# Kernel tuning notes

Measured on AMD Instinct MI355X. Metric: run time of the kernel, lower is better.

## Reference

```python
import jax, jax.numpy as jnp
import numpy as np

N_NODES = 100000
N_EDGES = 3200000


def setup_inputs() -> dict:
    key = jax.random.key(0)
    k1, k2, k3, k4 = jax.random.split(key, 4)
    x = jax.random.normal(k1, (N_NODES, 128), dtype=jnp.float32)
    edge_index = jax.random.randint(k2, (2, N_EDGES), 0, N_NODES, dtype=jnp.int64)
    W1 = jax.random.normal(k3, (128, 16), dtype=jnp.float32) * 0.1
    b1 = jnp.zeros((16,), dtype=jnp.float32)
    W2 = jax.random.normal(k4, (16, 1), dtype=jnp.float32) * 0.1
    b2 = jnp.zeros((1,), dtype=jnp.float32)
    return {"x": x, "edge_index": edge_index, "W1": W1, "b1": b1, "W2": W2, "b2": b2}


def _gcn_conv(h, row, col, norm, b, n):
    # message = h[src] * norm, scatter-add into dst (PyG source_to_target flow)
    msg = h[row] * norm[:, None]
    out = jax.ops.segment_sum(msg, col, num_segments=n)
    return out + b


def reference(x, edge_index, W1, b1, W2, b2):
    n = x.shape[0]
    loops = jnp.arange(n, dtype=edge_index.dtype)
    # GCN adds self-loops with weight 1
    row = jnp.concatenate([edge_index[0], loops])
    col = jnp.concatenate([edge_index[1], loops])
    ew = jnp.ones(row.shape[0], dtype=x.dtype)
    deg = jax.ops.segment_sum(ew, col, num_segments=n)
    dinv = jnp.where(deg > 0, deg ** -0.5, 0.0).astype(x.dtype)
    norm = dinv[row] * dinv[col]

    h = _gcn_conv(x @ W1, row, col, norm, b1, n)  # [N,16]
    h = jax.nn.relu(h)
    # dropout p=0.2 is identity in eval mode
    h = _gcn_conv(h @ W2, row, col, norm, b2, n)  # [N,1]
    return jax.nn.sigmoid(h).squeeze(-1)  # [N]
```

## Files before the change

### kernel.cpp

```cpp
#include <hip/hip_runtime.h>
#include <hip/hip_fp16.h>
#include <cstdint>


#define F_IN 128
#define F_HID 16
#define PB 1024
#define PT 8192
#define NBMAX 512
#define CAPMAX 15104

__global__ __launch_bounds__(PB) void partition_kernel(
    const int* __restrict__ row, const int* __restrict__ col,
    int* __restrict__ cursor,
    int* __restrict__ ping,
    int capB, int NB, int n_edges) {
    __shared__ int sh_hist[NBMAX];
    __shared__ int sh_scan[NBMAX];
    __shared__ int sh_cur[NBMAX];
    __shared__ int sh_base[NBMAX];
    __shared__ int sh_wsum[16];
    __shared__ int sh_packed[PT];
    __shared__ unsigned short sh_bkt[PT];

    int t = threadIdx.x;
    int lane = t & 63;
    int wv = t >> 6;
    int ntiles = (n_edges + PT - 1) / PT;
    bool vec_ok = ((n_edges & 3) == 0);

    for (int tile = blockIdx.x; tile < ntiles; tile += gridDim.x) {
        int tbase = tile * PT;
        int tcnt = min(PT, n_edges - tbase);

        if (t < NBMAX) sh_hist[t] = 0;
        __syncthreads();

        int e0 = tbase + t * 8;
        int pk[8], bb[8];
        if (vec_ok && e0 + 8 <= n_edges) {
            int4 a0 = *(const int4*)(row + e0);
            int4 a1 = *(const int4*)(row + e0 + 4);
            int4 c0 = *(const int4*)(col + e0);
            int4 c1 = *(const int4*)(col + e0 + 4);
            int rr[8] = {a0.x, a0.y, a0.z, a0.w, a1.x, a1.y, a1.z, a1.w};
            int cc[8] = {c0.x, c0.y, c0.z, c0.w, c1.x, c1.y, c1.z, c1.w};
#pragma unroll
            for (int k = 0; k < 8; k++) {
                bb[k] = cc[k] >> 8;
                pk[k] = rr[k] | ((cc[k] & 255) << 17);
                atomicAdd(&sh_hist[bb[k]], 1);
            }
        } else {
#pragma unroll
            for (int k = 0; k < 8; k++) {
                int e = e0 + k;
                bb[k] = -1;
                if (e < n_edges) {
                    int r = row[e];
                    int c = col[e];
                    bb[k] = c >> 8;
                    pk[k] = r | ((c & 255) << 17);
                    atomicAdd(&sh_hist[bb[k]], 1);
                }
            }
        }
        __syncthreads();

        {
            int v = (t < NBMAX) ? sh_hist[t] : 0;
            int incl = v;
#pragma unroll
            for (int off = 1; off < 64; off <<= 1) {
                int u = __shfl_up(incl, off, 64);
                if (lane >= off) incl += u;
            }
            if (lane == 63) sh_wsum[wv] = incl;
            __syncthreads();
            if (t < 16) {
                int s = sh_wsum[t];
#pragma unroll
                for (int off = 1; off < 16; off <<= 1) {
                    int u = __shfl_up(s, off, 16);
                    if (t >= off) s += u;
                }
                sh_wsum[t] = s;
            }
            __syncthreads();
            int wexcl = (wv > 0) ? sh_wsum[wv - 1] : 0;
            if (t < NBMAX) sh_scan[t] = incl + wexcl;
        }
        __syncthreads();

        if (t < NBMAX) {
            int h = sh_hist[t];
            sh_cur[t] = sh_scan[t] - h;
            sh_base[t] = (h > 0 && t < NB) ? atomicAdd(&cursor[t], h) : 0;
        }
        __syncthreads();

#pragma unroll
        for (int k = 0; k < 8; k++) {
            if (bb[k] >= 0) {
                int p = atomicAdd(&sh_cur[bb[k]], 1);
                sh_packed[p] = pk[k];
                sh_bkt[p] = (unsigned short)bb[k];
            }
        }
        __syncthreads();

#pragma unroll
        for (int k = 0; k < 8; k++) {
            int p = t + k * PB;
            if (p < tcnt) {
                int b = sh_bkt[p];
                int off = p - (sh_scan[b] - sh_hist[b]);
                int gp = sh_base[b] + off;
                if (gp < capB) ping[(size_t)b * capB + gp] = sh_packed[p];
            }
        }
        __syncthreads();
    }
}

__global__ __launch_bounds__(PB) void deg_gemm1_kernel(
    const int* __restrict__ cursor, const int* __restrict__ ping,
    const float* __restrict__ x, const float* __restrict__ W1,
    int* __restrict__ cnt, int* __restrict__ rowptr,
    __half* __restrict__ h1p, int capB, int n) {
    __shared__ float sW[F_IN * F_HID];
    __shared__ int hist[256];
    __shared__ int wsum[4];

    int b = blockIdx.x, t = threadIdx.x;
    int lane = t & 63;
    int wv = t >> 6;

    for (int i = t; i < F_IN * F_HID; i += PB) sW[i] = W1[i];
    if (t < 256) hist[t] = 0;
    __syncthreads();

    int cb = min(cursor[b], capB);
    const int* src = ping + (size_t)b * capB;
    for (int i = t; i < cb; i += PB) {
        atomicAdd(&hist[(src[i] >> 17) & 255], 1);
    }
    __syncthreads();

    {
        int h = (t < 256) ? hist[t] : 0;
        int incl = h;
#pragma unroll
        for (int off = 1; off < 64; off <<= 1) {
            int u = __shfl_up(incl, off, 64);
            if (lane >= off) incl += u;
        }
        if (t < 256 && lane == 63) wsum[wv] = incl;
        __syncthreads();
        if (t < 4) {
            int s = wsum[t];
#pragma unroll
            for (int off = 1; off < 4; off <<= 1) {
                int u = __shfl_up(s, off, 4);
                if (t >= off) s += u;
            }
            wsum[t] = s;
        }
        __syncthreads();
        if (t < 256) {
            int g = b * 256 + t;
            if (g < n) {
                int wexcl = (wv > 0) ? wsum[wv - 1] : 0;
                cnt[g] = h;
                rowptr[g] = b * capB + (incl + wexcl - h);
            }
        }
    }

    int sub = t >> 2;
    int node = b * 256 + sub;
    if (node >= n) return;
    int jq = (t & 3) * 4;

    const float4* xr = (const float4*)(x + (size_t)node * F_IN);
    float a0 = 0.0f, a1 = 0.0f, a2 = 0.0f, a3 = 0.0f;

#pragma unroll 4
    for (int k4 = 0; k4 < F_IN / 4; k4++) {
        float4 xv = xr[k4];
        const float* w0 = &sW[(k4 * 4 + 0) * F_HID + jq];
        const float* w1 = &sW[(k4 * 4 + 1) * F_HID + jq];
        const float* w2 = &sW[(k4 * 4 + 2) * F_HID + jq];
        const float* w3 = &sW[(k4 * 4 + 3) * F_HID + jq];
        a0 += xv.x * w0[0] + xv.y * w1[0] + xv.z * w2[0] + xv.w * w3[0];
        a1 += xv.x * w0[1] + xv.y * w1[1] + xv.z * w2[1] + xv.w * w3[1];
        a2 += xv.x * w0[2] + xv.y * w1[2] + xv.z * w2[2] + xv.w * w3[2];
        a3 += xv.x * w0[3] + xv.y * w1[3] + xv.z * w2[3] + xv.w * w3[3];
    }

    float d = rsqrtf((float)hist[sub] + 1.0f);
    __half2 hv[2];
    hv[0] = __floats2half2_rn(a0 * d, a1 * d);
    hv[1] = __floats2half2_rn(a2 * d, a3 * d);
    *(float2*)(h1p + (size_t)node * F_HID + jq) = *(float2*)&hv[0];
}

__global__ __launch_bounds__(PB) void sort_gather1(
    const int* __restrict__ cursor, const int* __restrict__ ping,
    const int* __restrict__ cnt, const int* __restrict__ rowptr,
    const __half* __restrict__ h1p, const float* __restrict__ b1,
    const float* __restrict__ W2, float* __restrict__ sp,
    int* __restrict__ pong, int capB, int n) {
    extern __shared__ int B[];
    __shared__ int s_excl[256];
    __shared__ int s_h[256];
    __shared__ int cur[256];

    int b = blockIdx.x, t = threadIdx.x;

    if (t < 256) {
        int g = b * 256 + t;
        int h = (g < n) ? cnt[g] : 0;
        int excl = (g < n) ? (rowptr[g] - b * capB) : 0;
        s_h[t] = h;
        s_excl[t] = excl;
        cur[t] = excl;
    }
    __syncthreads();

    int cb = min(cursor[b], capB);
    const int* src = ping + (size_t)b * capB;

    for (int i = t; i < cb; i += PB) {
        int v = src[i];
        int p = atomicAdd(&cur[(v >> 17) & 255], 1);
        B[p] = v & 131071;
    }
    __syncthreads();

    for (int i = t; i < cb; i += PB) {
        pong[(size_t)b * capB + i] = B[i];
    }

    int l = t & 7;
    for (int j = t >> 3; j < 256; j += (PB >> 3)) {
        int g = b * 256 + j;
        if (g >= n) continue;
        int h = s_h[j];
        int base = s_excl[j];
        int end = base + h;

        float ax = 0.0f, ay = 0.0f;
        for (; base + 8 <= end; base += 8) {
#pragma unroll
            for (int m = 0; m < 8; m++) {
                int rm = B[base + m];
                float2 f = __half22float2(*(const __half2*)(h1p + (size_t)rm * F_HID + 2 * l));
                ax += f.x; ay += f.y;
            }
        }
        for (int m = 0; m < end - base; m++) {
            int rm = B[base + m];
            float2 f = __half22float2(*(const __half2*)(h1p + (size_t)rm * F_HID + 2 * l));
            ax += f.x; ay += f.y;
        }

        float dc = rsqrtf((float)h + 1.0f);
        float2 fs = __half22float2(*(const __half2*)(h1p + (size_t)g * F_HID + 2 * l));
        float v0 = (ax + fs.x) * dc + b1[2 * l];
        float v1 = (ay + fs.y) * dc + b1[2 * l + 1];
        v0 = fmaxf(v0, 0.0f);
        v1 = fmaxf(v1, 0.0f);
        float tt = v0 * W2[2 * l] + v1 * W2[2 * l + 1];
        tt += __shfl_xor(tt, 1, 8);
        tt += __shfl_xor(tt, 2, 8);
        tt += __shfl_xor(tt, 4, 8);
        if (l == 0) sp[g] = tt * dc;
    }
}

__global__ __launch_bounds__(256) void gather2_kernel(const int* __restrict__ rowptr,
                                                      const int* __restrict__ cnt,
                                                      const int* __restrict__ eidx,
                                                      const float* __restrict__ sp,
                                                      const float* __restrict__ b2,
                                                      float* __restrict__ out, int n) {
    int g = (blockIdx.x * 256 + threadIdx.x) >> 4;
    int lane = threadIdx.x & 15;
    if (g >= n) return;
    int start = rowptr[g];
    int end = start + cnt[g];

    float acc = 0.0f;
    for (int e = start + lane; e < end; e += 16) {
        acc += sp[eidx[e]];
    }
    acc += __shfl_xor(acc, 1, 16);
    acc += __shfl_xor(acc, 2, 16);
    acc += __shfl_xor(acc, 4, 16);
    acc += __shfl_xor(acc, 8, 16);
    if (lane == 0) {
        float v = (acc + sp[g]) * rsqrtf((float)cnt[g] + 1.0f) + b2[0];
        out[g] = 1.0f / (1.0f + __expf(-v));
    }
}

__global__ void bucket_scatter_kernel(const int* __restrict__ row,
                                      const int* __restrict__ col,
                                      int* __restrict__ cnt,
                                      int* __restrict__ eidx,
                                      int cap, int n_edges) {
    int e = blockIdx.x * blockDim.x + threadIdx.x;
    if (e < n_edges) {
        int c = col[e];
        int p = atomicAdd(&cnt[c], 1);
        if (p < cap) eidx[(size_t)c * cap + p] = row[e];
    }
}

__global__ __launch_bounds__(256) void gemm1f_kernel(const float* __restrict__ x,
                                                     const float* __restrict__ W1,
                                                     const int* __restrict__ cnt,
                                                     float* __restrict__ h1p, int n) {
    __shared__ float sW[F_IN * F_HID];
    int tid = threadIdx.x;
    for (int i = tid; i < F_IN * F_HID; i += 256) sW[i] = W1[i];
    __syncthreads();
    int node = blockIdx.x * 256 + tid;
    if (node >= n) return;
    const float4* xr = (const float4*)(x + (size_t)node * F_IN);
    float acc[F_HID];
#pragma unroll
    for (int j = 0; j < F_HID; j++) acc[j] = 0.0f;
#pragma unroll 4
    for (int k4 = 0; k4 < F_IN / 4; k4++) {
        float4 xv = xr[k4];
        const float* w0 = &sW[(k4 * 4 + 0) * F_HID];
        const float* w1 = &sW[(k4 * 4 + 1) * F_HID];
        const float* w2 = &sW[(k4 * 4 + 2) * F_HID];
        const float* w3 = &sW[(k4 * 4 + 3) * F_HID];
#pragma unroll
        for (int j = 0; j < F_HID; j++) {
            acc[j] += xv.x * w0[j] + xv.y * w1[j] + xv.z * w2[j] + xv.w * w3[j];
        }
    }
    float d = rsqrtf((float)cnt[node] + 1.0f);
    float4* outp = (float4*)(h1p + (size_t)node * F_HID);
    outp[0] = make_float4(acc[0] * d, acc[1] * d, acc[2] * d, acc[3] * d);
    outp[1] = make_float4(acc[4] * d, acc[5] * d, acc[6] * d, acc[7] * d);
    outp[2] = make_float4(acc[8] * d, acc[9] * d, acc[10] * d, acc[11] * d);
    outp[3] = make_float4(acc[12] * d, acc[13] * d, acc[14] * d, acc[15] * d);
}

__global__ __launch_bounds__(256) void fb_gather1_kernel(const int* __restrict__ cnt,
                                                         const int* __restrict__ eidx,
                                                         const float* __restrict__ h1p,
                                                         const float* __restrict__ b1,
                                                         const float* __restrict__ W2,
                                                         float* __restrict__ sp,
                                                         int cap, int n) {
    int g = (blockIdx.x * 256 + threadIdx.x) >> 4;
    int lane = threadIdx.x & 15;
    if (g >= n) return;
    int start = g * cap;
    int end = start + min(cnt[g], cap);
    float acc = 0.0f;
    for (int base = start; base < end; base += 16) {
        int e = base + lane;
        int r = (e < end) ? eidx[e] : 0;
        int m_cnt = min(16, end - base);
        for (int m = 0; m < m_cnt; m++) {
            int rm = __shfl(r, m, 16);
            acc += h1p[(size_t)rm * F_HID + lane];
        }
    }
    float dc = rsqrtf((float)cnt[g] + 1.0f);
    float v = (acc + h1p[(size_t)g * F_HID + lane]) * dc + b1[lane];
    v = fmaxf(v, 0.0f);
    float t = v * W2[lane];
    t += __shfl_xor(t, 1, 16);
    t += __shfl_xor(t, 2, 16);
    t += __shfl_xor(t, 4, 16);
    t += __shfl_xor(t, 8, 16);
    if (lane == 0) sp[g] = t * dc;
}

__global__ __launch_bounds__(256) void fb_gather2_kernel(const int* __restrict__ cnt,
                                                         const int* __restrict__ eidx,
                                                         const float* __restrict__ sp,
                                                         const float* __restrict__ b2,
                                                         float* __restrict__ out,
                                                         int cap, int n) {
    int g = (blockIdx.x * 256 + threadIdx.x) >> 4;
    int lane = threadIdx.x & 15;
    if (g >= n) return;
    int start = g * cap;
    int end = start + min(cnt[g], cap);
    float acc = 0.0f;
    for (int e = start + lane; e < end; e += 16) {
        acc += sp[eidx[e]];
    }
    acc += __shfl_xor(acc, 1, 16);
    acc += __shfl_xor(acc, 2, 16);
    acc += __shfl_xor(acc, 4, 16);
    acc += __shfl_xor(acc, 8, 16);
    if (lane == 0) {
        float v = (acc + sp[g]) * rsqrtf((float)cnt[g] + 1.0f) + b2[0];
        out[g] = 1.0f / (1.0f + __expf(-v));
    }
}

extern "C" void kernel_launch(void* const* d_in, const int* in_sizes, int n_in,
                              void* d_out, int out_size, void* d_ws, size_t ws_size,
                              hipStream_t stream) {
    const float* x  = (const float*)d_in[0];
    const int*   ei = (const int*)d_in[1];
    const float* W1 = (const float*)d_in[2];
    const float* b1 = (const float*)d_in[3];
    const float* W2 = (const float*)d_in[4];
    const float* b2 = (const float*)d_in[5];
    float* out = (float*)d_out;

    const int n = in_sizes[0] / F_IN;
    const int n_edges = in_sizes[1] / 2;
    const int* row = ei;
    const int* col = ei + n_edges;

    const size_t S = ((size_t)n + 511) & ~(size_t)511;
    const size_t words = ws_size / 4;

    const int B = 256;
    const int gridE = (n_edges + B - 1) / B;
    const int gridN = (n + B - 1) / B;

    const int NB = (n + 255) >> 8;
    int meanB = (NB > 0) ? (n_edges / NB) : 0;
    int capB = ((meanB + meanB / 8 + 1024) + 15) & ~15;
    size_t need_new = 11 * S + (size_t)NBMAX + 2 * (size_t)NB * (size_t)capB;

    if (n <= 131072 && NB <= NBMAX && capB <= CAPMAX && words >= need_new) {
        int*    cnt    = (int*)d_ws;
        int*    cursor = cnt + S;
        int*    rowptr = cursor + NBMAX;
        float*  sp     = (float*)(rowptr + S);
        __half* h1p    = (__half*)(sp + S);
        int*    ping   = (int*)(sp + S) + 8 * S;
        int*    pong   = ping + (size_t)NB * capB;

        hipMemsetAsync(cursor, 0, NBMAX * sizeof(int), stream);
        int ntiles = (n_edges + PT - 1) / PT;
        int pgrid = min(2048, ntiles);
        partition_kernel<<<pgrid, PB, 0, stream>>>(row, col, cursor, ping,
                                                   capB, NB, n_edges);
        deg_gemm1_kernel<<<NB, PB, 0, stream>>>(cursor, ping, x, W1, cnt,
                                                rowptr, h1p, capB, n);
        sort_gather1<<<NB, PB, (size_t)capB * sizeof(int), stream>>>(
            cursor, ping, cnt, rowptr, h1p, b1, W2, sp, pong, capB, n);
        int gridG2 = (n * 16 + B - 1) / B;
        gather2_kernel<<<gridG2, B, 0, stream>>>(rowptr, cnt, pong, sp, b2, out, n);
    } else {
        int*   cnt  = (int*)d_ws;
        float* sp   = (float*)(cnt + S);
        float* h1pf = sp + S;
        int*   eidx = (int*)(h1pf + 16 * S);
        size_t tail_words = (words > 18 * S) ? (words - 18 * S) : 0;
        int cap = (int)min((size_t)96, tail_words / (size_t)(n > 0 ? n : 1));
        const int gridG = (n * 16 + B - 1) / B;

        hipMemsetAsync(cnt, 0, (size_t)n * sizeof(int), stream);
        bucket_scatter_kernel<<<gridE, B, 0, stream>>>(row, col, cnt, eidx, cap, n_edges);
        gemm1f_kernel<<<gridN, B, 0, stream>>>(x, W1, cnt, h1pf, n);
        fb_gather1_kernel<<<gridG, B, 0, stream>>>(cnt, eidx, h1pf, b1, W2, sp, cap, n);
        fb_gather2_kernel<<<gridG, B, 0, stream>>>(cnt, eidx, sp, b2, out, cap, n);
    }
}
```

Measured before the change: 178.3 us.

## Fuse layer-1 gather and layer-2 gather into one cooperative kernel with grid sync

Combines the sort/gather for layer 1 and the gather for layer 2 into a single cooperative kernel that keeps the per-bucket sorted source indices in shared memory across a grid-wide barrier. This avoids writing and re-reading the pong index array and saves a kernel launch. Layer 2 then reads the sorted indices straight from LDS. The kernel needs every block of the grid (NB blocks of 1024 threads with large dynamic LDS) to be resident at once, and falls back to the two-kernel path if the cooperative launch fails.

Measured after the change: 353.7 us. 1.98x slower.

```diff
diff --git a/kernel.cpp b/kernel.cpp
--- a/kernel.cpp
+++ b/kernel.cpp
@@ -1,6 +1,9 @@
 #include <hip/hip_runtime.h>
 #include <hip/hip_fp16.h>
+#include <hip/hip_cooperative_groups.h>
 #include <cstdint>
+
+namespace cg = cooperative_groups;
 
 
 #define F_IN 128
@@ -203,6 +206,102 @@
     hv[0] = __floats2half2_rn(a0 * d, a1 * d);
     hv[1] = __floats2half2_rn(a2 * d, a3 * d);
     *(float2*)(h1p + (size_t)node * F_HID + jq) = *(float2*)&hv[0];
+}
+
+__global__ __launch_bounds__(PB) void sort_gather12(
+    const int* __restrict__ cursor, const int* __restrict__ ping,
+    const int* __restrict__ cnt, const int* __restrict__ rowptr,
+    const __half* __restrict__ h1p, const float* __restrict__ b1,
+    const float* __restrict__ W2, float* __restrict__ sp,
+    const float* __restrict__ b2, float* __restrict__ out,
+    int capB, int n) {
+    extern __shared__ int B[];
+    __shared__ int s_excl[256];
+    __shared__ int s_h[256];
+    __shared__ int cur[256];
+
+    int b = blockIdx.x, t = threadIdx.x;
+
+    if (t < 256) {
+        int g = b * 256 + t;
+        int h = (g < n) ? cnt[g] : 0;
+        int excl = (g < n) ? (rowptr[g] - b * capB) : 0;
+        s_h[t] = h;
+        s_excl[t] = excl;
+        cur[t] = excl;
+    }
+    __syncthreads();
+
+    int cb = min(cursor[b], capB);
+    const int* src = ping + (size_t)b * capB;
+
+    for (int i = t; i < cb; i += PB) {
+        int v = src[i];
+        int p = atomicAdd(&cur[(v >> 17) & 255], 1);
+        B[p] = v & 131071;
+    }
+    __syncthreads();
+
+    int l = t & 7;
+    for (int j = t >> 3; j < 256; j += (PB >> 3)) {
+        int g = b * 256 + j;
+        if (g >= n) continue;
+        int h = s_h[j];
+        int base = s_excl[j];
+        int end = base + h;
+
+        float ax = 0.0f, ay = 0.0f;
+        for (; base + 8 <= end; base += 8) {
+#pragma unroll
+            for (int m = 0; m < 8; m++) {
+                int rm = B[base + m];
+                float2 f = __half22float2(*(const __half2*)(h1p + (size_t)rm * F_HID + 2 * l));
+                ax += f.x; ay += f.y;
+            }
+        }
+        for (int m = 0; m < end - base; m++) {
+            int rm = B[base + m];
+            float2 f = __half22float2(*(const __half2*)(h1p + (size_t)rm * F_HID + 2 * l));
+            ax += f.x; ay += f.y;
+        }
+
+        float dc = rsqrtf((float)h + 1.0f);
+        float2 fs = __half22float2(*(const __half2*)(h1p + (size_t)g * F_HID + 2 * l));
+        float v0 = (ax + fs.x) * dc + b1[2 * l];
+        float v1 = (ay + fs.y) * dc + b1[2 * l + 1];
+        v0 = fmaxf(v0, 0.0f);
+        v1 = fmaxf(v1, 0.0f);
+        float tt = v0 * W2[2 * l] + v1 * W2[2 * l + 1];
+        tt += __shfl_xor(tt, 1, 8);
+        tt += __shfl_xor(tt, 2, 8);
+        tt += __shfl_xor(tt, 4, 8);
+        if (l == 0) sp[g] = tt * dc;
+    }
+
+    __threadfence();
+    cg::this_grid().sync();
+
+    int l16 = t & 15;
+    for (int j = t >> 4; j < 256; j += (PB >> 4)) {
+        int g = b * 256 + j;
+        if (g >= n) continue;
+        int h = s_h[j];
+        int base = s_excl[j];
+        int end = base + h;
+
+        float acc = 0.0f;
+        for (int e = base + l16; e < end; e += 16) {
+            acc += sp[B[e]];
+        }
+        acc += __shfl_xor(acc, 1, 16);
+        acc += __shfl_xor(acc, 2, 16);
+        acc += __shfl_xor(acc, 4, 16);
+        acc += __shfl_xor(acc, 8, 16);
+        if (l16 == 0) {
+            float v = (acc + sp[g]) * rsqrtf((float)h + 1.0f) + b2[0];
+            out[g] = 1.0f / (1.0f + __expf(-v));
+        }
+    }
 }
 
 __global__ __launch_bounds__(PB) void sort_gather1(
@@ -454,10 +553,27 @@
                                                    capB, NB, n_edges);
         deg_gemm1_kernel<<<NB, PB, 0, stream>>>(cursor, ping, x, W1, cnt,
                                                 rowptr, h1p, capB, n);
-        sort_gather1<<<NB, PB, (size_t)capB * sizeof(int), stream>>>(
-            cursor, ping, cnt, rowptr, h1p, b1, W2, sp, pong, capB, n);
-        int gridG2 = (n * 16 + B - 1) / B;
-        gather2_kernel<<<gridG2, B, 0, stream>>>(rowptr, cnt, pong, sp, b2, out, n);
+
+        {
+            const int*    a_cursor = cursor;  const int* a_ping = ping;
+            const int*    a_cnt = cnt;        const int* a_rowptr = rowptr;
+            const __half* a_h1p = h1p;        const float* a_b1 = b1;
+            const float*  a_W2 = W2;          float* a_sp = sp;
+            const float*  a_b2 = b2;          float* a_out = out;
+            int a_capB = capB;                int a_n = n;
+            void* args[] = {&a_cursor, &a_ping, &a_cnt, &a_rowptr, &a_h1p,
+                            &a_b1, &a_W2, &a_sp, &a_b2, &a_out, &a_capB, &a_n};
+            hipError_t cerr = hipLaunchCooperativeKernel(
+                (void*)sort_gather12, dim3(NB), dim3(PB), args,
+                (size_t)capB * sizeof(int), stream);
+            if (cerr != hipSuccess) {
+                sort_gather1<<<NB, PB, (size_t)capB * sizeof(int), stream>>>(
+                    cursor, ping, cnt, rowptr, h1p, b1, W2, sp, pong, capB, n);
+                int gridG2 = (n * 16 + B - 1) / B;
+                gather2_kernel<<<gridG2, B, 0, stream>>>(rowptr, cnt, pong, sp,
+                                                         b2, out, n);
+            }
+        }
     } else {
         int*   cnt  = (int*)d_ws;
         float* sp   = (float*)(cnt + S);
```
